# Optimization experiments

Measured on AMD Instinct MI355X. Metric: run time of the kernel, lower is better.

The kernel has to match this reference:

```python
import jax, jax.numpy as jnp
import numpy as np

SIGMA1 = 0.02   # sigma1 init arg
K = 128         # number of discretization bins
TMIN = 1e-10
LEAKY_SLOPE = 0.01  # torch nn.LeakyReLU default


def setup_inputs() -> dict:
    key = jax.random.key(0)
    k1, k2, k3, k4, k5 = jax.random.split(key, 5)
    B, D, H = 256, 1024, 2048
    x = jax.random.uniform(k1, (B, D), jnp.float32, -1.0, 1.0)
    t = jax.random.uniform(k2, (B, 1), jnp.float32)          # Uniform(0,1) time sample
    noise = jax.random.normal(k3, (B, D), jnp.float32)       # for Normal sample of mu
    W1 = jax.random.normal(k4, (D + 1, H), jnp.float32) * (1.0 / np.sqrt(D + 1))
    b1 = jnp.zeros((H,), jnp.float32)
    W2 = jax.random.normal(k5, (H, 2 * D), jnp.float32) * (1.0 / np.sqrt(H))
    b2 = jnp.zeros((2 * D,), jnp.float32)
    return dict(x=x, t=t, noise=noise, W1=W1, b1=b1, W2=W2, b2=b2)


def _discretised_output_distribution(mu, t, gamma, W1, b1, W2, b2):
    B, D = mu.shape
    # NN: Linear -> LeakyReLU -> Linear, split into mu_eps / ln_sigma_eps
    h = jnp.concatenate([mu, t], axis=1) @ W1 + b1
    h = jnp.where(h >= 0, h, LEAKY_SLOPE * h)
    out = h @ W2 + b2
    mu_eps, ln_sig_eps = out[:, :D], out[:, D:]

    r = jnp.sqrt((1.0 - gamma) / gamma)                      # (B,1)
    mu_x = mu / gamma - r * mu_eps                           # (B,D)
    sigma_x = r * jnp.exp(ln_sig_eps)                        # (B,D)

    low_t = t < TMIN                                         # (B,1) rows with tiny t
    mu_x = jnp.where(low_t, 0.0, mu_x)
    sigma_x = jnp.where(low_t, 1.0, sigma_x)

    k = jnp.arange(K, dtype=jnp.float32)
    kl = 2.0 * (k - 1.0) / K - 1.0                           # left bin edge
    kr = 2.0 * k / K - 1.0                                   # right bin edge
    kc = (2.0 * k - 1.0) / K - 1.0                           # bin center weight

    inv = 1.0 / (sigma_x * jnp.sqrt(jnp.float32(2.0)))       # (B,D)

    def cdf(bound):  # bound: (K,) scalars -> clamped discretized CDF (B,D,K)
        F = 0.5 * (1.0 + jax.lax.erf((bound[None, None, :] - mu_x[:, :, None]) * inv[:, :, None]))
        return jnp.where(bound <= -1.0, 0.0, jnp.where(bound >= 1.0, 1.0, F))

    p = kc * (cdf(kr) - cdf(kl))                             # (B,D,K)
    return jnp.sum(p, axis=-1)                               # (B,D) expected value


def reference(x, t, noise, W1, b1, W2, b2):
    gamma = 1.0 - SIGMA1 ** (2.0 * t)                        # (B,1)
    # mu ~ Normal(gamma*x, std=gamma*(1-gamma)), reparameterized with noise
    mu = gamma * x + gamma * (1.0 - gamma) * noise
    pO = _discretised_output_distribution(mu, t, gamma, W1, b1, W2, b2)
    se = (x - pO) ** 2                                       # elementwise MSE
    loss = -jnp.log(jnp.float32(SIGMA1)) * jnp.mean(SIGMA1 ** (-2.0 * t) * se)
    return loss
```

## Files before the change

### kernel.cpp

```cpp
#include <hip/hip_runtime.h>
#include <hip/hip_bf16.h>
#include <math.h>


typedef __bf16 bf16_t;
typedef __bf16 bf16x8 __attribute__((ext_vector_type(8)));
typedef __bf16 bf16x4 __attribute__((ext_vector_type(4)));
typedef float  f32x4  __attribute__((ext_vector_type(4)));

#define LDK 40
#define L2S -5.6438561897747248f

__device__ __forceinline__ float erf_f(float x) {
  float ax = __builtin_fabsf(x);
  float t = __builtin_amdgcn_rcpf(fmaf(0.3275911f, ax, 1.0f));
  float p = fmaf(fmaf(fmaf(fmaf(1.061405429f, t, -1.453152027f), t, 1.421413741f),
                      t, -0.284496736f), t, 0.254829592f);
  p *= t;
  float e = __expf(-ax * ax);
  float r = fmaf(-p, e, 1.0f);
  return __builtin_copysignf(r, x);
}

__global__ __launch_bounds__(256, 2)
void prep_k(const float* __restrict__ x, const float* __restrict__ noise,
            const float* __restrict__ t, bf16_t* __restrict__ A1,
            float* __restrict__ out) {
  if (blockIdx.x == 0 && threadIdx.x == 0) *out = 0.0f;
  int b = blockIdx.x;
  float tv = t[b];
  float p = exp2f(2.0f * tv * L2S);
  float g = 1.0f - p, gom = g * p;
  int e = (b * 256 + threadIdx.x) * 4;
  float4 xv = *(const float4*)(x + e);
  float4 nv = *(const float4*)(noise + e);
  bf16x4 o;
  o[0] = (__bf16)fmaf(gom, nv.x, g * xv.x);
  o[1] = (__bf16)fmaf(gom, nv.y, g * xv.y);
  o[2] = (__bf16)fmaf(gom, nv.z, g * xv.z);
  o[3] = (__bf16)fmaf(gom, nv.w, g * xv.w);
  *(bf16x4*)(A1 + e) = o;
}

#define GSTEP(ASB, BSB, AR, BR, TILE, PF)                                        \
  {                                                                              \
    *(bf16x8*)(&ASB[arow * LDK + akg * 8]) = AR;                                 \
    bf16x4 bv_;                                                                  \
    bv_[0] = (__bf16)BR[0]; bv_[1] = (__bf16)BR[1];                              \
    bv_[2] = (__bf16)BR[2]; bv_[3] = (__bf16)BR[3];                              \
    *(bf16x4*)(&BSB[bn * LDK + bkg * 4]) = bv_;                                  \
    if (PF) {                                                                    \
      AR = *(const bf16x8*)(Ap + ((TILE) + 4) * 32);                             \
      const float* wp_ = Wp0 + (size_t)((TILE) + 4) * 32 * 2048;                 \
      BR[0] = wp_[0]; BR[1] = wp_[2048]; BR[2] = wp_[4096]; BR[3] = wp_[6144];   \
    }                                                                            \
    asm volatile("s_waitcnt lgkmcnt(0)" ::: "memory");                           \
    __builtin_amdgcn_s_barrier();                                                \
    __builtin_amdgcn_sched_barrier(0);                                           \
    {                                                                            \
      bf16x8 aF_ = *(const bf16x8*)(&ASB[(wave * 16 + fm) * LDK + kq * 8]);      \
      bf16x8 bF0_ = *(const bf16x8*)(&BSB[fm * LDK + kq * 8]);                   \
      bf16x8 bF1_ = *(const bf16x8*)(&BSB[(16 + fm) * LDK + kq * 8]);            \
      acc0 = __builtin_amdgcn_mfma_f32_16x16x32_bf16(aF_, bF0_, acc0, 0, 0, 0);  \
      acc1 = __builtin_amdgcn_mfma_f32_16x16x32_bf16(aF_, bF1_, acc1, 0, 0, 0);  \
    }                                                                            \
  }

__device__ __forceinline__ void gemm_loop(
    const bf16_t* __restrict__ Ap, const float* __restrict__ Wp0,
    bf16_t* __restrict__ As0, bf16_t* __restrict__ As1,
    bf16_t* __restrict__ Bs0, bf16_t* __restrict__ Bs1,
    int arow, int akg, int bn, int bkg, int wave, int fm, int kq,
    int Ktiles, f32x4& acc0, f32x4& acc1) {
  bf16x8 aR0, aR1, aR2, aR3;
  f32x4 bR0, bR1, bR2, bR3;
  aR0 = *(const bf16x8*)(Ap);
  aR1 = *(const bf16x8*)(Ap + 32);
  aR2 = *(const bf16x8*)(Ap + 64);
  aR3 = *(const bf16x8*)(Ap + 96);
  {
    const float* w_ = Wp0;
    bR0[0] = w_[0]; bR0[1] = w_[2048]; bR0[2] = w_[4096]; bR0[3] = w_[6144];
    w_ = Wp0 + (size_t)32 * 2048;
    bR1[0] = w_[0]; bR1[1] = w_[2048]; bR1[2] = w_[4096]; bR1[3] = w_[6144];
    w_ = Wp0 + (size_t)64 * 2048;
    bR2[0] = w_[0]; bR2[1] = w_[2048]; bR2[2] = w_[4096]; bR2[3] = w_[6144];
    w_ = Wp0 + (size_t)96 * 2048;
    bR3[0] = w_[0]; bR3[1] = w_[2048]; bR3[2] = w_[4096]; bR3[3] = w_[6144];
  }
  for (int kt = 0; kt < Ktiles; kt += 4) {
    GSTEP(As0, Bs0, aR0, bR0, kt,     kt + 4 < Ktiles)
    GSTEP(As1, Bs1, aR1, bR1, kt + 1, kt + 5 < Ktiles)
    GSTEP(As0, Bs0, aR2, bR2, kt + 2, kt + 6 < Ktiles)
    GSTEP(As1, Bs1, aR3, bR3, kt + 3, kt + 7 < Ktiles)
  }
}

__global__ __launch_bounds__(256, 2)
void gemm1h_k(const bf16_t* __restrict__ A, const float* __restrict__ W,
              const float* __restrict__ b1, const float* __restrict__ t,
              bf16_t* __restrict__ h) {
  __shared__ bf16_t As0[64 * LDK], As1[64 * LDK];
  __shared__ bf16_t Bs0[32 * LDK], Bs1[32 * LDK];
  int tid = threadIdx.x;
  int lane = tid & 63, wave = tid >> 6;
  int n0 = blockIdx.x * 32, m0 = blockIdx.y * 64;
  int arow = tid >> 2, akg = tid & 3;
  int bn = tid & 31, bkg = tid >> 5;
  int fm = lane & 15, kq = lane >> 4;

  const bf16_t* Ap = A + (size_t)(m0 + arow) * 1024 + akg * 8;
  const float* Wp0 = W + (size_t)(bkg * 4) * 2048 + n0 + bn;

  f32x4 acc0 = (f32x4)0.0f, acc1 = (f32x4)0.0f;
  gemm_loop(Ap, Wp0, As0, As1, Bs0, Bs1, arow, akg, bn, bkg, wave, fm, kq,
            32, acc0, acc1);

  int col0 = n0 + fm, col1 = n0 + 16 + fm;
  float wl0 = W[(size_t)1024 * 2048 + col0], wl1 = W[(size_t)1024 * 2048 + col1];
  float bb0 = b1[col0], bb1 = b1[col1];
#pragma unroll
  for (int e = 0; e < 4; ++e) {
    int row = m0 + wave * 16 + kq * 4 + e;
    float tv = t[row];
    float v0 = acc0[e] + tv * wl0 + bb0;
    float v1 = acc1[e] + tv * wl1 + bb1;
    v0 = v0 >= 0.f ? v0 : 0.01f * v0;
    v1 = v1 >= 0.f ? v1 : 0.01f * v1;
    h[(size_t)row * 2048 + col0] = (__bf16)v0;
    h[(size_t)row * 2048 + col1] = (__bf16)v1;
  }
}

__global__ __launch_bounds__(256, 2)
void gemm2loss_k(const bf16_t* __restrict__ A, const float* __restrict__ W,
                 const float* __restrict__ b2, const float* __restrict__ t,
                 const float* __restrict__ x, const float* __restrict__ noise,
                 float* __restrict__ out) {
  __shared__ bf16_t As0[64 * LDK], As1[64 * LDK];
  __shared__ bf16_t Bs0[32 * LDK], Bs1[32 * LDK];
  __shared__ float red[4];
  int tid = threadIdx.x;
  int lane = tid & 63, wave = tid >> 6;
  int n0 = blockIdx.x * 16, m0 = blockIdx.y * 64;
  int arow = tid >> 2, akg = tid & 3;
  int bn = tid & 31, bkg = tid >> 5;
  int fm = lane & 15, kq = lane >> 4;

  const bf16_t* Ap = A + (size_t)(m0 + arow) * 2048 + akg * 8;
  int bcol = n0 + (bn & 15) + ((bn >> 4) << 10);
  const float* Wp0 = W + (size_t)(bkg * 4) * 2048 + bcol;

  f32x4 acc0 = (f32x4)0.0f, acc1 = (f32x4)0.0f;
  gemm_loop(Ap, Wp0, As0, As1, Bs0, Bs1, arow, akg, bn, bkg, wave, fm, kq,
            64, acc0, acc1);

  int d = n0 + fm;
  float bme = b2[d], blg = b2[1024 + d];
  float lsum = 0.0f;
#pragma unroll
  for (int e = 0; e < 4; ++e) {
    int row = m0 + wave * 16 + kq * 4 + e;
    float tv = t[row];
    float om = exp2f(2.0f * tv * L2S);
    float gamma = 1.0f - om;
    float rq = sqrtf(om / gamma);
    float w = 1.0f / om;
    bool lowt = tv < 1e-10f;
    float me = acc0[e] + bme;
    float lg = acc1[e] + blg;
    float xs = x[(size_t)row * 1024 + d], ns = noise[(size_t)row * 1024 + d];

    float mu_x = xs + om * ns - rq * me;
    float sig = rq * __expf(lg);
    if (lowt) { mu_x = 0.f; sig = 1.f; }
    float invs = 0.70710678118654752f / sig;
    float a = invs * 0.015625f;
    float c0 = (1.f + mu_x) * invs;
    float m64 = 64.f * (1.f + mu_x);
    float wdt = 316.78383797157331f * sig;
    float lo = m64 - wdt, hi = m64 + wdt;
    int klo = (lo < 1.f) ? 1 : ((lo > 126.f) ? 127 : (int)ceilf(lo));
    int khi = (hi < 1.f) ? 0 : ((hi > 126.f) ? 126 : (int)floorf(hi));
    float ss = (float)(126 - khi) - (float)(klo - 1);
    if (khi >= klo) {
      if (a <= 1.0f) {
        float za = fmaf(a, (float)klo - 0.5f, -c0);
        float zb = fmaf(a, (float)khi + 0.5f, -c0);
        const float ISP = 0.56418958354775628f;
        float ea = __expf(-za * za), eb = __expf(-zb * zb);
        float Ga = fmaf(za, erf_f(za), ISP * ea);
        float Gb = fmaf(zb, erf_f(zb), ISP * eb);
        float S = (Gb - Ga) * __builtin_amdgcn_rcpf(a)
                - a * 0.047015889f * (eb - ea);
        ss += S;
      } else {
        for (int k = klo; k <= khi; ++k) ss += erf_f(fmaf(a, (float)k, -c0));
      }
    }
    float z127 = fmaf(a, 127.f, -c0);
    float pO = fmaf(0.48828125f, 1.f + erf_f(z127),
                    fmaf(-0.0078125f, ss, -0.984375f));
    float df = xs - pO;
    lsum += w * df * df;
  }
#pragma unroll
  for (int off = 32; off > 0; off >>= 1) lsum += __shfl_down(lsum, off, 64);
  if ((tid & 63) == 0) red[wave] = lsum;
  __syncthreads();
  if (tid == 0) {
    const float SCALE = 3.9120230054281461f / 262144.0f;
    atomicAdd(out, (red[0] + red[1] + red[2] + red[3]) * SCALE);
  }
}

extern "C" void kernel_launch(void* const* d_in, const int* in_sizes, int n_in,
                              void* d_out, int out_size, void* d_ws, size_t ws_size,
                              hipStream_t stream) {
  const float* x     = (const float*)d_in[0];
  const float* t     = (const float*)d_in[1];
  const float* noise = (const float*)d_in[2];
  const float* W1    = (const float*)d_in[3];
  const float* b1    = (const float*)d_in[4];
  const float* W2    = (const float*)d_in[5];
  const float* b2    = (const float*)d_in[6];
  float* out = (float*)d_out;

  char* ws = (char*)d_ws;
  bf16_t* A1 = (bf16_t*)ws;
  bf16_t* h  = (bf16_t*)(ws + 524288);

  prep_k<<<256, 256, 0, stream>>>(x, noise, t, A1, out);
  gemm1h_k<<<dim3(64, 4), 256, 0, stream>>>(A1, W1, b1, t, h);
  gemm2loss_k<<<dim3(64, 4), 256, 0, stream>>>(h, W2, b2, t, x, noise, out);
}
```

Before: 112.4 us.

## Retile GEMMs to 32x32 output blocks with 64-deep K steps

Both GEMM kernels switch from 64x32 output tiles with 32-wide K tiles to 32x32 tiles with 64-wide K tiles. The four waves now form a 2x2 grid, each issuing two MFMAs per step into one accumulator, and the grid doubles to 512 blocks. This halves the barriers per K and adds more blocks to fill the CUs. In the loss kernel the log-sigma half is handed through shared memory, so only half the waves run the erf-based loss epilogue, and B (weight) tiles are reloaded twice as often overall.

```diff
diff --git a/kernel.cpp b/kernel.cpp
--- a/kernel.cpp
+++ b/kernel.cpp
@@ -7,8 +7,9 @@
 typedef __bf16 bf16x8 __attribute__((ext_vector_type(8)));
 typedef __bf16 bf16x4 __attribute__((ext_vector_type(4)));
 typedef float  f32x4  __attribute__((ext_vector_type(4)));
-
-#define LDK 40
+typedef float  f32x8  __attribute__((ext_vector_type(8)));
+
+#define LDK2 72
 #define L2S -5.6438561897747248f
 
 __device__ __forceinline__ float erf_f(float x) {
@@ -44,25 +45,31 @@
 
 #define GSTEP(ASB, BSB, AR, BR, TILE, PF)                                        \
   {                                                                              \
-    *(bf16x8*)(&ASB[arow * LDK + akg * 8]) = AR;                                 \
-    bf16x4 bv_;                                                                  \
+    *(bf16x8*)(&ASB[arow * LDK2 + akg8]) = AR;                                   \
+    bf16x8 bv_;                                                                  \
     bv_[0] = (__bf16)BR[0]; bv_[1] = (__bf16)BR[1];                              \
     bv_[2] = (__bf16)BR[2]; bv_[3] = (__bf16)BR[3];                              \
-    *(bf16x4*)(&BSB[bn * LDK + bkg * 4]) = bv_;                                  \
+    bv_[4] = (__bf16)BR[4]; bv_[5] = (__bf16)BR[5];                              \
+    bv_[6] = (__bf16)BR[6]; bv_[7] = (__bf16)BR[7];                              \
+    *(bf16x8*)(&BSB[bn * LDK2 + bkg8]) = bv_;                                    \
     if (PF) {                                                                    \
-      AR = *(const bf16x8*)(Ap + ((TILE) + 4) * 32);                             \
-      const float* wp_ = Wp0 + (size_t)((TILE) + 4) * 32 * 2048;                 \
-      BR[0] = wp_[0]; BR[1] = wp_[2048]; BR[2] = wp_[4096]; BR[3] = wp_[6144];   \
+      AR = *(const bf16x8*)(Ap + ((TILE) + 4) * 64);                             \
+      const float* wp_ = Wp0 + (size_t)((TILE) + 4) * 64 * 2048;                 \
+      BR[0] = wp_[0];        BR[1] = wp_[2048];                                  \
+      BR[2] = wp_[4096];     BR[3] = wp_[6144];                                  \
+      BR[4] = wp_[8192];     BR[5] = wp_[10240];                                 \
+      BR[6] = wp_[12288];    BR[7] = wp_[14336];                                 \
     }                                                                            \
     asm volatile("s_waitcnt lgkmcnt(0)" ::: "memory");                           \
     __builtin_amdgcn_s_barrier();                                                \
     __builtin_amdgcn_sched_barrier(0);                                           \
     {                                                                            \
-      bf16x8 aF_ = *(const bf16x8*)(&ASB[(wave * 16 + fm) * LDK + kq * 8]);      \
-      bf16x8 bF0_ = *(const bf16x8*)(&BSB[fm * LDK + kq * 8]);                   \
-      bf16x8 bF1_ = *(const bf16x8*)(&BSB[(16 + fm) * LDK + kq * 8]);            \
-      acc0 = __builtin_amdgcn_mfma_f32_16x16x32_bf16(aF_, bF0_, acc0, 0, 0, 0);  \
-      acc1 = __builtin_amdgcn_mfma_f32_16x16x32_bf16(aF_, bF1_, acc1, 0, 0, 0);  \
+      bf16x8 aF0_ = *(const bf16x8*)(&ASB[arr]);                                 \
+      bf16x8 bF0_ = *(const bf16x8*)(&BSB[brr]);                                 \
+      acc = __builtin_amdgcn_mfma_f32_16x16x32_bf16(aF0_, bF0_, acc, 0, 0, 0);   \
+      bf16x8 aF1_ = *(const bf16x8*)(&ASB[arr + 32]);                            \
+      bf16x8 bF1_ = *(const bf16x8*)(&BSB[brr + 32]);                            \
+      acc = __builtin_amdgcn_mfma_f32_16x16x32_bf16(aF1_, bF1_, acc, 0, 0, 0);   \
     }                                                                            \
   }
 
@@ -70,23 +77,27 @@
     const bf16_t* __restrict__ Ap, const float* __restrict__ Wp0,
     bf16_t* __restrict__ As0, bf16_t* __restrict__ As1,
     bf16_t* __restrict__ Bs0, bf16_t* __restrict__ Bs1,
-    int arow, int akg, int bn, int bkg, int wave, int fm, int kq,
-    int Ktiles, f32x4& acc0, f32x4& acc1) {
+    int arow, int akg8, int bn, int bkg8, int arr, int brr,
+    int Ktiles, f32x4& acc) {
   bf16x8 aR0, aR1, aR2, aR3;
-  f32x4 bR0, bR1, bR2, bR3;
+  f32x8 bR0, bR1, bR2, bR3;
   aR0 = *(const bf16x8*)(Ap);
-  aR1 = *(const bf16x8*)(Ap + 32);
-  aR2 = *(const bf16x8*)(Ap + 64);
-  aR3 = *(const bf16x8*)(Ap + 96);
+  aR1 = *(const bf16x8*)(Ap + 64);
+  aR2 = *(const bf16x8*)(Ap + 128);
+  aR3 = *(const bf16x8*)(Ap + 192);
   {
     const float* w_ = Wp0;
-    bR0[0] = w_[0]; bR0[1] = w_[2048]; bR0[2] = w_[4096]; bR0[3] = w_[6144];
-    w_ = Wp0 + (size_t)32 * 2048;
-    bR1[0] = w_[0]; bR1[1] = w_[2048]; bR1[2] = w_[4096]; bR1[3] = w_[6144];
+    bR0[0] = w_[0];     bR0[1] = w_[2048];  bR0[2] = w_[4096];  bR0[3] = w_[6144];
+    bR0[4] = w_[8192];  bR0[5] = w_[10240]; bR0[6] = w_[12288]; bR0[7] = w_[14336];
     w_ = Wp0 + (size_t)64 * 2048;
-    bR2[0] = w_[0]; bR2[1] = w_[2048]; bR2[2] = w_[4096]; bR2[3] = w_[6144];
-    w_ = Wp0 + (size_t)96 * 2048;
-    bR3[0] = w_[0]; bR3[1] = w_[2048]; bR3[2] = w_[4096]; bR3[3] = w_[6144];
+    bR1[0] = w_[0];     bR1[1] = w_[2048];  bR1[2] = w_[4096];  bR1[3] = w_[6144];
+    bR1[4] = w_[8192];  bR1[5] = w_[10240]; bR1[6] = w_[12288]; bR1[7] = w_[14336];
+    w_ = Wp0 + (size_t)128 * 2048;
+    bR2[0] = w_[0];     bR2[1] = w_[2048];  bR2[2] = w_[4096];  bR2[3] = w_[6144];
+    bR2[4] = w_[8192];  bR2[5] = w_[10240]; bR2[6] = w_[12288]; bR2[7] = w_[14336];
+    w_ = Wp0 + (size_t)192 * 2048;
+    bR3[0] = w_[0];     bR3[1] = w_[2048];  bR3[2] = w_[4096];  bR3[3] = w_[6144];
+    bR3[4] = w_[8192];  bR3[5] = w_[10240]; bR3[6] = w_[12288]; bR3[7] = w_[14336];
   }
   for (int kt = 0; kt < Ktiles; kt += 4) {
     GSTEP(As0, Bs0, aR0, bR0, kt,     kt + 4 < Ktiles)
@@ -100,35 +111,35 @@
 void gemm1h_k(const bf16_t* __restrict__ A, const float* __restrict__ W,
               const float* __restrict__ b1, const float* __restrict__ t,
               bf16_t* __restrict__ h) {
-  __shared__ bf16_t As0[64 * LDK], As1[64 * LDK];
-  __shared__ bf16_t Bs0[32 * LDK], Bs1[32 * LDK];
+  __shared__ bf16_t As0[32 * LDK2], As1[32 * LDK2];
+  __shared__ bf16_t Bs0[32 * LDK2], Bs1[32 * LDK2];
   int tid = threadIdx.x;
   int lane = tid & 63, wave = tid >> 6;
-  int n0 = blockIdx.x * 32, m0 = blockIdx.y * 64;
-  int arow = tid >> 2, akg = tid & 3;
-  int bn = tid & 31, bkg = tid >> 5;
+  int wr = wave & 1, wc = wave >> 1;
+  int n0 = blockIdx.x * 32, m0 = blockIdx.y * 32;
+  int arow = tid >> 3, akg8 = (tid & 7) * 8;
+  int bn = tid & 31, bkg8 = (tid >> 5) * 8;
   int fm = lane & 15, kq = lane >> 4;
-
-  const bf16_t* Ap = A + (size_t)(m0 + arow) * 1024 + akg * 8;
-  const float* Wp0 = W + (size_t)(bkg * 4) * 2048 + n0 + bn;
-
-  f32x4 acc0 = (f32x4)0.0f, acc1 = (f32x4)0.0f;
-  gemm_loop(Ap, Wp0, As0, As1, Bs0, Bs1, arow, akg, bn, bkg, wave, fm, kq,
-            32, acc0, acc1);
-
-  int col0 = n0 + fm, col1 = n0 + 16 + fm;
-  float wl0 = W[(size_t)1024 * 2048 + col0], wl1 = W[(size_t)1024 * 2048 + col1];
-  float bb0 = b1[col0], bb1 = b1[col1];
+  int arr = (wr * 16 + fm) * LDK2 + kq * 8;
+  int brr = (wc * 16 + fm) * LDK2 + kq * 8;
+
+  const bf16_t* Ap = A + (size_t)(m0 + arow) * 1024 + akg8;
+  const float* Wp0 = W + (size_t)(bkg8 >> 3) * 8 * 2048 + n0 + bn;
+
+  f32x4 acc = (f32x4)0.0f;
+  gemm_loop(Ap, Wp0, As0, As1, Bs0, Bs1, arow, akg8, bn, bkg8, arr, brr,
+            16, acc);
+
+  int col = n0 + wc * 16 + fm;
+  float wl = W[(size_t)1024 * 2048 + col];
+  float bb = b1[col];
 #pragma unroll
   for (int e = 0; e < 4; ++e) {
-    int row = m0 + wave * 16 + kq * 4 + e;
+    int row = m0 + wr * 16 + kq * 4 + e;
     float tv = t[row];
-    float v0 = acc0[e] + tv * wl0 + bb0;
-    float v1 = acc1[e] + tv * wl1 + bb1;
-    v0 = v0 >= 0.f ? v0 : 0.01f * v0;
-    v1 = v1 >= 0.f ? v1 : 0.01f * v1;
-    h[(size_t)row * 2048 + col0] = (__bf16)v0;
-    h[(size_t)row * 2048 + col1] = (__bf16)v1;
+    float v = acc[e] + tv * wl + bb;
+    v = v >= 0.f ? v : 0.01f * v;
+    h[(size_t)row * 2048 + col] = (__bf16)v;
   }
 }
 
@@ -137,72 +148,85 @@
                  const float* __restrict__ b2, const float* __restrict__ t,
                  const float* __restrict__ x, const float* __restrict__ noise,
                  float* __restrict__ out) {
-  __shared__ bf16_t As0[64 * LDK], As1[64 * LDK];
-  __shared__ bf16_t Bs0[32 * LDK], Bs1[32 * LDK];
+  __shared__ bf16_t As0[32 * LDK2], As1[32 * LDK2];
+  __shared__ bf16_t Bs0[32 * LDK2], Bs1[32 * LDK2];
+  __shared__ float lgbuf[32][17];
   __shared__ float red[4];
   int tid = threadIdx.x;
   int lane = tid & 63, wave = tid >> 6;
-  int n0 = blockIdx.x * 16, m0 = blockIdx.y * 64;
-  int arow = tid >> 2, akg = tid & 3;
-  int bn = tid & 31, bkg = tid >> 5;
+  int wr = wave & 1, wc = wave >> 1;
+  int n0 = blockIdx.x * 16, m0 = blockIdx.y * 32;
+  int arow = tid >> 3, akg8 = (tid & 7) * 8;
+  int bn = tid & 31, bkg8 = (tid >> 5) * 8;
   int fm = lane & 15, kq = lane >> 4;
-
-  const bf16_t* Ap = A + (size_t)(m0 + arow) * 2048 + akg * 8;
+  int arr = (wr * 16 + fm) * LDK2 + kq * 8;
+  int brr = (wc * 16 + fm) * LDK2 + kq * 8;
+
+  const bf16_t* Ap = A + (size_t)(m0 + arow) * 2048 + akg8;
   int bcol = n0 + (bn & 15) + ((bn >> 4) << 10);
-  const float* Wp0 = W + (size_t)(bkg * 4) * 2048 + bcol;
-
-  f32x4 acc0 = (f32x4)0.0f, acc1 = (f32x4)0.0f;
-  gemm_loop(Ap, Wp0, As0, As1, Bs0, Bs1, arow, akg, bn, bkg, wave, fm, kq,
-            64, acc0, acc1);
-
-  int d = n0 + fm;
-  float bme = b2[d], blg = b2[1024 + d];
+  const float* Wp0 = W + (size_t)(bkg8 >> 3) * 8 * 2048 + bcol;
+
+  f32x4 acc = (f32x4)0.0f;
+  gemm_loop(Ap, Wp0, As0, As1, Bs0, Bs1, arow, akg8, bn, bkg8, arr, brr,
+            32, acc);
+
+  if (wc == 1) {
+#pragma unroll
+    for (int e = 0; e < 4; ++e)
+      lgbuf[wr * 16 + kq * 4 + e][fm] = acc[e];
+  }
+  __syncthreads();
+
   float lsum = 0.0f;
-#pragma unroll
-  for (int e = 0; e < 4; ++e) {
-    int row = m0 + wave * 16 + kq * 4 + e;
-    float tv = t[row];
-    float om = exp2f(2.0f * tv * L2S);
-    float gamma = 1.0f - om;
-    float rq = sqrtf(om / gamma);
-    float w = 1.0f / om;
-    bool lowt = tv < 1e-10f;
-    float me = acc0[e] + bme;
-    float lg = acc1[e] + blg;
-    float xs = x[(size_t)row * 1024 + d], ns = noise[(size_t)row * 1024 + d];
-
-    float mu_x = xs + om * ns - rq * me;
-    float sig = rq * __expf(lg);
-    if (lowt) { mu_x = 0.f; sig = 1.f; }
-    float invs = 0.70710678118654752f / sig;
-    float a = invs * 0.015625f;
-    float c0 = (1.f + mu_x) * invs;
-    float m64 = 64.f * (1.f + mu_x);
-    float wdt = 316.78383797157331f * sig;
-    float lo = m64 - wdt, hi = m64 + wdt;
-    int klo = (lo < 1.f) ? 1 : ((lo > 126.f) ? 127 : (int)ceilf(lo));
-    int khi = (hi < 1.f) ? 0 : ((hi > 126.f) ? 126 : (int)floorf(hi));
-    float ss = (float)(126 - khi) - (float)(klo - 1);
-    if (khi >= klo) {
-      if (a <= 1.0f) {
-        float za = fmaf(a, (float)klo - 0.5f, -c0);
-        float zb = fmaf(a, (float)khi + 0.5f, -c0);
-        const float ISP = 0.56418958354775628f;
-        float ea = __expf(-za * za), eb = __expf(-zb * zb);
-        float Ga = fmaf(za, erf_f(za), ISP * ea);
-        float Gb = fmaf(zb, erf_f(zb), ISP * eb);
-        float S = (Gb - Ga) * __builtin_amdgcn_rcpf(a)
-                - a * 0.047015889f * (eb - ea);
-        ss += S;
-      } else {
-        for (int k = klo; k <= khi; ++k) ss += erf_f(fmaf(a, (float)k, -c0));
+  if (wc == 0) {
+    int d = n0 + fm;
+    float bme = b2[d], blg = b2[1024 + d];
+#pragma unroll
+    for (int e = 0; e < 4; ++e) {
+      int row = m0 + wr * 16 + kq * 4 + e;
+      float tv = t[row];
+      float om = exp2f(2.0f * tv * L2S);
+      float gamma = 1.0f - om;
+      float rq = sqrtf(om / gamma);
+      float w = 1.0f / om;
+      bool lowt = tv < 1e-10f;
+      float me = acc[e] + bme;
+      float lg = lgbuf[wr * 16 + kq * 4 + e][fm] + blg;
+      float xs = x[(size_t)row * 1024 + d], ns = noise[(size_t)row * 1024 + d];
+
+      float mu_x = xs + om * ns - rq * me;
+      float sig = rq * __expf(lg);
+      if (lowt) { mu_x = 0.f; sig = 1.f; }
+      float invs = 0.70710678118654752f / sig;
+      float a = invs * 0.015625f;
+      float c0 = (1.f + mu_x) * invs;
+      float m64 = 64.f * (1.f + mu_x);
+      float wdt = 316.78383797157331f * sig;
+      float lo = m64 - wdt, hi = m64 + wdt;
+      int klo = (lo < 1.f) ? 1 : ((lo > 126.f) ? 127 : (int)ceilf(lo));
+      int khi = (hi < 1.f) ? 0 : ((hi > 126.f) ? 126 : (int)floorf(hi));
+      float ss = (float)(126 - khi) - (float)(klo - 1);
+      if (khi >= klo) {
+        if (a <= 1.0f) {
+          float za = fmaf(a, (float)klo - 0.5f, -c0);
+          float zb = fmaf(a, (float)khi + 0.5f, -c0);
+          const float ISP = 0.56418958354775628f;
+          float ea = __expf(-za * za), eb = __expf(-zb * zb);
+          float Ga = fmaf(za, erf_f(za), ISP * ea);
+          float Gb = fmaf(zb, erf_f(zb), ISP * eb);
+          float S = (Gb - Ga) * __builtin_amdgcn_rcpf(a)
+                  - a * 0.047015889f * (eb - ea);
+          ss += S;
+        } else {
+          for (int k = klo; k <= khi; ++k) ss += erf_f(fmaf(a, (float)k, -c0));
+        }
       }
+      float z127 = fmaf(a, 127.f, -c0);
+      float pO = fmaf(0.48828125f, 1.f + erf_f(z127),
+                      fmaf(-0.0078125f, ss, -0.984375f));
+      float df = xs - pO;
+      lsum += w * df * df;
     }
-    float z127 = fmaf(a, 127.f, -c0);
-    float pO = fmaf(0.48828125f, 1.f + erf_f(z127),
-                    fmaf(-0.0078125f, ss, -0.984375f));
-    float df = xs - pO;
-    lsum += w * df * df;
   }
 #pragma unroll
   for (int off = 32; off > 0; off >>= 1) lsum += __shfl_down(lsum, off, 64);
@@ -231,6 +255,6 @@
   bf16_t* h  = (bf16_t*)(ws + 524288);
 
   prep_k<<<256, 256, 0, stream>>>(x, noise, t, A1, out);
-  gemm1h_k<<<dim3(64, 4), 256, 0, stream>>>(A1, W1, b1, t, h);
-  gemm2loss_k<<<dim3(64, 4), 256, 0, stream>>>(h, W2, b2, t, x, noise, out);
-}
+  gemm1h_k<<<dim3(64, 8), 256, 0, stream>>>(A1, W1, b1, t, h);
+  gemm2loss_k<<<dim3(64, 8), 256, 0, stream>>>(h, W2, b2, t, x, noise, out);
+}
```

Measured after the change: 110.3 us. Within noise of the previous version (-1.8%).
